# Kernel optimization log

Hardware: AMD Instinct MI355X
Metric: run time of the kernel (lower is better)

The kernel has to match this reference:

```python
import jax, jax.numpy as jnp
import numpy as np
from jax import lax

SOFTPLUS_THRESHOLD = 20.0

def _softplus_thresh(z):
    # softplus(z, beta=1, threshold=20): linear above threshold
    return jnp.where(z > SOFTPLUS_THRESHOLD, z,
                     jnp.log1p(jnp.exp(jnp.minimum(z, SOFTPLUS_THRESHOLD))))

def setup_inputs() -> dict:
    key = jax.random.key(0)
    ks = jax.random.split(key, 8)
    L, E, R, N = 512, 5120, 160, 16
    scale = 0.02
    x = jax.random.normal(ks[0], (1, 1, L, E), dtype=jnp.float32)
    W_dt_low = jax.random.normal(ks[1], (E, R), dtype=jnp.float32) * scale
    W_dt = jax.random.normal(ks[2], (R, E), dtype=jnp.float32) * scale
    dt_bias = jax.random.normal(ks[3], (E,), dtype=jnp.float32) * scale
    W_B = jax.random.normal(ks[4], (E, N), dtype=jnp.float32) * scale
    W_C = jax.random.normal(ks[5], (E, N), dtype=jnp.float32) * scale
    # A_log ~ log of positive values so A = -exp(A_log) is a stable decay
    A_log = jnp.log(1.0 + jax.random.uniform(ks[6], (E, N), dtype=jnp.float32) * 15.0)
    D = jax.random.normal(ks[7], (E,), dtype=jnp.float32)
    return {"x": x, "W_dt_low": W_dt_low, "W_dt": W_dt, "dt_bias": dt_bias,
            "W_B": W_B, "W_C": W_C, "A_log": A_log, "D": D}

def reference(x, W_dt_low, W_dt, dt_bias, W_B, W_C, A_log, D):
    orig_shape = x.shape              # [1,1,L,E]
    L, E = orig_shape[-2], orig_shape[-1]
    xf = x.reshape(L, E)
    # delta_t: x -> dt_rank -> d_inner, then thresholded softplus
    delta = _softplus_thresh((xf @ W_dt_low) @ W_dt + dt_bias)   # [L,E]
    A = -jnp.exp(A_log)                                          # [E,N]
    # discretization: abar = exp(delta * A), bbar = delta * B * x
    abar = jnp.exp(delta[:, :, None] * A[None])                  # [L,E,N]
    B = xf @ W_B                                                 # [L,N]
    bbar = delta[:, :, None] * B[:, None, :] * xf[:, :, None]    # [L,E,N]
    # linear recurrence h_t = abar_t * h_{t-1} + bbar_t via associative scan
    def combine(c1, c2):
        a1, b1 = c1
        a2, b2 = c2
        return a1 * a2, a2 * b1 + b2
    _, h = lax.associative_scan(combine, (abar, bbar), axis=0)   # [L,E,N]
    C = xf @ W_C                                                 # [L,N]
    y = jnp.einsum('len,ln->le', h, C)                           # hc_sum_reduce
    out = xf * D + y
    return out.reshape(orig_shape)
```

## Files before the change

### kernel.cpp

```cpp
#include <hip/hip_runtime.h>
#include <math.h>

#define LL 512
#define EE 5120
#define RR 160
#define NS 16
#define NTOT 192
#define KS 32
#define KCHUNK 160
#define CH 16
#define NC 32

#define XCONV_BLOCKS 1280
#define WALL_TILES   960
#define WDT_TILES    800

typedef __attribute__((ext_vector_type(8))) short short8;
typedef __attribute__((ext_vector_type(4))) short short4v;
typedef __attribute__((ext_vector_type(4))) float f32x4;

__device__ inline float softplus_t(float z) {
    return z > 20.f ? z : log1pf(__expf(fminf(z, 20.f)));
}

__device__ inline short f2bf(float f) {
    unsigned u = __float_as_uint(f);
    unsigned r = (u + 0x7FFFu + ((u >> 16) & 1u)) >> 16;
    return (short)r;
}

__device__ inline float bf2f(unsigned short u) {
    return __uint_as_float(((unsigned)u) << 16);
}

__global__ __launch_bounds__(256) void prep_kernel(
        const float* __restrict__ x,
        const float* __restrict__ Wlow,
        const float* __restrict__ WB,
        const float* __restrict__ WC,
        const float* __restrict__ Wdt,
        short* __restrict__ xb,
        short* __restrict__ WallT,
        short* __restrict__ WdtT) {
    const int tid = threadIdx.x;
    const int bid = blockIdx.x;
    if (bid < XCONV_BLOCKS) {
        size_t base = (size_t)bid * 2048 + (size_t)tid * 8;
        float4 v0 = *reinterpret_cast<const float4*>(x + base);
        float4 v1 = *reinterpret_cast<const float4*>(x + base + 4);
        short8 o;
        o[0] = f2bf(v0.x); o[1] = f2bf(v0.y); o[2] = f2bf(v0.z); o[3] = f2bf(v0.w);
        o[4] = f2bf(v1.x); o[5] = f2bf(v1.y); o[6] = f2bf(v1.z); o[7] = f2bf(v1.w);
        *reinterpret_cast<short8*>(xb + base) = o;
        return;
    }
    __shared__ float tile[32][33];
    const int row = tid >> 3, col4 = (tid & 7) * 4;
    if (bid < XCONV_BLOCKS + WALL_TILES) {
        const int t = bid - XCONV_BLOCKS;
        const int k0 = (t / 6) * 32, n0 = (t % 6) * 32;
#pragma unroll
        for (int i = 0; i < 4; ++i) {
            int n = n0 + col4 + i, k = k0 + row;
            float v;
            if (n < RR)            v = Wlow[(size_t)k * RR + n];
            else if (n < RR + NS)  v = WB[(size_t)k * NS + (n - RR)];
            else                   v = WC[(size_t)k * NS + (n - RR - NS)];
            tile[row][col4 + i] = v;
        }
        __syncthreads();
        const int nr = tid >> 3, kc = (tid & 7) * 4;
        short4v o;
#pragma unroll
        for (int i = 0; i < 4; ++i) o[i] = f2bf(tile[kc + i][nr]);
        *reinterpret_cast<short4v*>(WallT + (size_t)(n0 + nr) * EE + k0 + kc) = o;
    } else {
        const int t = bid - XCONV_BLOCKS - WALL_TILES;
        const int n0 = (t / 5) * 32, k0 = (t % 5) * 32;
#pragma unroll
        for (int i = 0; i < 4; ++i)
            tile[row][col4 + i] = Wdt[(size_t)(k0 + row) * EE + n0 + col4 + i];
        __syncthreads();
        const int nr = tid >> 3, kc = (tid & 7) * 4;
        short4v o;
#pragma unroll
        for (int i = 0; i < 4; ++i) o[i] = f2bf(tile[kc + i][nr]);
        *reinterpret_cast<short4v*>(WdtT + (size_t)(n0 + nr) * RR + k0 + kc) = o;
    }
}

__global__ __launch_bounds__(256) void g1m_kernel(
        const short* __restrict__ xb,
        const short* __restrict__ WallT,
        float* __restrict__ part) {
    const int tid = threadIdx.x;
    const int w = tid >> 6, l = tid & 63;
    const int wm = w >> 1, wn = w & 1;
    const int m0 = blockIdx.x * 64 + wm * 32;
    const int n0 = blockIdx.y * 64 + wn * 32;
    const int kz = blockIdx.z;
    const int row16 = l & 15, kg = (l >> 4) * 8;
    f32x4 acc[2][2] = {};
    const short* ap0 = xb + (size_t)(m0 + row16) * EE + kz * KCHUNK + kg;
    const short* ap1 = ap0 + (size_t)16 * EE;
    const short* bp0 = WallT + (size_t)(n0 + row16) * EE + kz * KCHUNK + kg;
    const short* bp1 = bp0 + (size_t)16 * EE;
#pragma unroll
    for (int s = 0; s < KCHUNK / 32; ++s) {
        short8 a0 = *reinterpret_cast<const short8*>(ap0 + s * 32);
        short8 a1 = *reinterpret_cast<const short8*>(ap1 + s * 32);
        short8 b0 = *reinterpret_cast<const short8*>(bp0 + s * 32);
        short8 b1 = *reinterpret_cast<const short8*>(bp1 + s * 32);
        acc[0][0] = __builtin_amdgcn_mfma_f32_16x16x32_bf16(a0, b0, acc[0][0], 0, 0, 0);
        acc[0][1] = __builtin_amdgcn_mfma_f32_16x16x32_bf16(a0, b1, acc[0][1], 0, 0, 0);
        acc[1][0] = __builtin_amdgcn_mfma_f32_16x16x32_bf16(a1, b0, acc[1][0], 0, 0, 0);
        acc[1][1] = __builtin_amdgcn_mfma_f32_16x16x32_bf16(a1, b1, acc[1][1], 0, 0, 0);
    }
    const int r0 = (l >> 4) * 4;
    const int c = l & 15;
#pragma unroll
    for (int i = 0; i < 2; ++i)
#pragma unroll
        for (int j = 0; j < 2; ++j) {
            size_t base = ((size_t)kz * LL + (m0 + i * 16 + r0)) * NTOT + (n0 + j * 16 + c);
            part[base]            = acc[i][j][0];
            part[base + NTOT]     = acc[i][j][1];
            part[base + 2 * NTOT] = acc[i][j][2];
            part[base + 3 * NTOT] = acc[i][j][3];
        }
}

__global__ __launch_bounds__(256) void r1_kernel(
        const float* __restrict__ part,
        short* __restrict__ tmpb,
        float* __restrict__ Bb,
        float* __restrict__ Cb) {
    int idx = blockIdx.x * 256 + threadIdx.x;
    int m = idx / NTOT, j = idx % NTOT;
    float s = 0.f;
#pragma unroll
    for (int ks = 0; ks < KS; ++ks) s += part[(size_t)ks * LL * NTOT + idx];
    if (j < RR) tmpb[m * RR + j] = f2bf(s);
    else if (j < RR + NS) Bb[m * NS + (j - RR)] = s;
    else Cb[m * NS + (j - RR - NS)] = s;
}

__global__ __launch_bounds__(256) void g2m_kernel(
        const short* __restrict__ tmpb,
        const short* __restrict__ WdtT,
        const float* __restrict__ bias,
        unsigned short* __restrict__ deltab) {
    const int tid = threadIdx.x;
    const int w = tid >> 6, l = tid & 63;
    const int wm = w >> 1, wn = w & 1;
    const int m0 = blockIdx.x * 64 + wm * 32;
    const int n0 = blockIdx.y * 64 + wn * 32;
    const int row16 = l & 15, koff = (l >> 4) * 8;
    f32x4 acc[2][2] = {};
    const short* aptr0 = tmpb + (size_t)(m0 + row16) * RR + koff;
    const short* aptr1 = aptr0 + (size_t)16 * RR;
    const short* bptr0 = WdtT + (size_t)(n0 + row16) * RR + koff;
    const short* bptr1 = bptr0 + (size_t)16 * RR;
#pragma unroll
    for (int s = 0; s < 5; ++s) {
        short8 a0 = *reinterpret_cast<const short8*>(aptr0 + s * 32);
        short8 a1 = *reinterpret_cast<const short8*>(aptr1 + s * 32);
        short8 b0 = *reinterpret_cast<const short8*>(bptr0 + s * 32);
        short8 b1 = *reinterpret_cast<const short8*>(bptr1 + s * 32);
        acc[0][0] = __builtin_amdgcn_mfma_f32_16x16x32_bf16(a0, b0, acc[0][0], 0, 0, 0);
        acc[0][1] = __builtin_amdgcn_mfma_f32_16x16x32_bf16(a0, b1, acc[0][1], 0, 0, 0);
        acc[1][0] = __builtin_amdgcn_mfma_f32_16x16x32_bf16(a1, b0, acc[1][0], 0, 0, 0);
        acc[1][1] = __builtin_amdgcn_mfma_f32_16x16x32_bf16(a1, b1, acc[1][1], 0, 0, 0);
    }
    const int r0 = (l >> 4) * 4;
    const int c = l & 15;
#pragma unroll
    for (int i = 0; i < 2; ++i) {
        int m = m0 + i * 16 + r0;
#pragma unroll
        for (int j = 0; j < 2; ++j) {
            int n = n0 + j * 16 + c;
            float bv = bias[n];
#pragma unroll
            for (int r = 0; r < 4; ++r)
                deltab[(size_t)(m + r) * EE + n] =
                    (unsigned short)f2bf(softplus_t(acc[i][j][r] + bv));
        }
    }
}

__global__ __launch_bounds__(256) void passA_kernel(
        const unsigned short* __restrict__ deltab,
        const unsigned short* __restrict__ xb,
        const float* __restrict__ Bb,
        const float* __restrict__ A_log,
        unsigned short* __restrict__ Hloc,
        float* __restrict__ sumd) {
    __shared__ float b_lds[CH][NS];
    const int c = blockIdx.y;
    const int e = blockIdx.x * 256 + threadIdx.x;
    const int t0 = c * CH;
    for (int v = threadIdx.x; v < CH * NS; v += 256)
        b_lds[v >> 4][v & 15] = Bb[t0 * NS + v];
    __syncthreads();

    float Ac[NS];
#pragma unroll
    for (int q = 0; q < 4; ++q) {
        float4 al = *reinterpret_cast<const float4*>(&A_log[(size_t)e * NS + q * 4]);
        Ac[q * 4 + 0] = -__expf(al.x);
        Ac[q * 4 + 1] = -__expf(al.y);
        Ac[q * 4 + 2] = -__expf(al.z);
        Ac[q * 4 + 3] = -__expf(al.w);
    }
    float h[NS];
#pragma unroll
    for (int n = 0; n < NS; ++n) h[n] = 0.f;
    float sd = 0.f;

#pragma unroll
    for (int tt = 0; tt < CH; ++tt) {
        float d  = bf2f(deltab[(size_t)(t0 + tt) * EE + e]);
        float xv = bf2f(xb[(size_t)(t0 + tt) * EE + e]);
        sd += d;
        float bx = d * xv;
#pragma unroll
        for (int n = 0; n < NS; ++n) {
            float a = __expf(d * Ac[n]);
            h[n] = a * h[n] + bx * b_lds[tt][n];
        }
    }
    size_t base = ((size_t)c * EE + e) * NS;
    short8 p0, p1;
#pragma unroll
    for (int n = 0; n < 8; ++n) { p0[n] = f2bf(h[n]); p1[n] = f2bf(h[n + 8]); }
    *reinterpret_cast<short8*>(Hloc + base)     = p0;
    *reinterpret_cast<short8*>(Hloc + base + 8) = p1;
    sumd[(size_t)c * EE + e] = sd;
}

__global__ __launch_bounds__(256) void passB_kernel(
        const unsigned short* __restrict__ Hloc,
        const float* __restrict__ sumd,
        const float* __restrict__ A_log,
        unsigned short* __restrict__ Hstart) {
    const int wk = blockIdx.x * 256 + threadIdx.x;
    const int eB = wk >> 4;
    const float AcB = -__expf(A_log[wk]);
    float hs = 0.f;
#pragma unroll
    for (int cc = 0; cc < NC; ++cc) {
        size_t off = (size_t)cc * EE * NS + wk;
        Hstart[off] = (unsigned short)f2bf(hs);
        hs = __expf(AcB * sumd[(size_t)cc * EE + eB]) * hs + bf2f(Hloc[off]);
    }
}

__global__ __launch_bounds__(256) void passC_kernel(
        const unsigned short* __restrict__ deltab,
        const unsigned short* __restrict__ xb,
        const float* __restrict__ Bb,
        const float* __restrict__ Cb,
        const float* __restrict__ A_log,
        const float* __restrict__ Dvec,
        const unsigned short* __restrict__ Hstart,
        float* __restrict__ out) {
    __shared__ float b_lds[CH][NS];
    __shared__ float c_lds[CH][NS];
    const int c = blockIdx.y;
    const int e = blockIdx.x * 256 + threadIdx.x;
    const int t0 = c * CH;
    for (int v = threadIdx.x; v < CH * NS; v += 256) {
        b_lds[v >> 4][v & 15] = Bb[t0 * NS + v];
        c_lds[v >> 4][v & 15] = Cb[t0 * NS + v];
    }
    __syncthreads();

    float Ac[NS];
#pragma unroll
    for (int q = 0; q < 4; ++q) {
        float4 al = *reinterpret_cast<const float4*>(&A_log[(size_t)e * NS + q * 4]);
        Ac[q * 4 + 0] = -__expf(al.x);
        Ac[q * 4 + 1] = -__expf(al.y);
        Ac[q * 4 + 2] = -__expf(al.z);
        Ac[q * 4 + 3] = -__expf(al.w);
    }
    float h[NS];
    size_t base = ((size_t)c * EE + e) * NS;
    {
        short8 p0 = *reinterpret_cast<const short8*>(Hstart + base);
        short8 p1 = *reinterpret_cast<const short8*>(Hstart + base + 8);
#pragma unroll
        for (int n = 0; n < 8; ++n) {
            h[n]     = bf2f((unsigned short)p0[n]);
            h[n + 8] = bf2f((unsigned short)p1[n]);
        }
    }
    const float Dval = Dvec[e];

#pragma unroll
    for (int tt = 0; tt < CH; ++tt) {
        float d  = bf2f(deltab[(size_t)(t0 + tt) * EE + e]);
        float xv = bf2f(xb[(size_t)(t0 + tt) * EE + e]);
        float bx = d * xv;
        float y = 0.f;
#pragma unroll
        for (int n = 0; n < NS; ++n) {
            float a = __expf(d * Ac[n]);
            h[n] = a * h[n] + bx * b_lds[tt][n];
            y += h[n] * c_lds[tt][n];
        }
        out[(size_t)(t0 + tt) * EE + e] = xv * Dval + y;
    }
}

extern "C" void kernel_launch(void* const* d_in, const int* in_sizes, int n_in,
                              void* d_out, int out_size, void* d_ws, size_t ws_size,
                              hipStream_t stream) {
    const float* x     = (const float*)d_in[0];
    const float* Wlow  = (const float*)d_in[1];
    const float* Wdt   = (const float*)d_in[2];
    const float* bias  = (const float*)d_in[3];
    const float* WB    = (const float*)d_in[4];
    const float* WC    = (const float*)d_in[5];
    const float* Alog  = (const float*)d_in[6];
    const float* Dv    = (const float*)d_in[7];
    float* out = (float*)d_out;
    float* wsf = (float*)d_ws;

    float*          Bb     = wsf;
    float*          Cb     = wsf + 8192;
    short*          WallT  = (short*)(wsf + 16384);
    short*          WdtT   = (short*)(wsf + 507904);
    short*          tmpb   = (short*)(wsf + 917504);
    short*          xb     = (short*)(wsf + 958464);
    float*          part   = wsf + 2269184;
    unsigned short* deltab = (unsigned short*)(wsf + 5414912);
    unsigned short* Hloc   = (unsigned short*)(wsf + 6725632);
    unsigned short* Hstart = (unsigned short*)(wsf + 8036352);
    float*          sumd   = wsf + 9347072;

    prep_kernel<<<dim3(XCONV_BLOCKS + WALL_TILES + WDT_TILES), 256, 0, stream>>>(
        x, Wlow, WB, WC, Wdt, xb, WallT, WdtT);
    g1m_kernel<<<dim3(8, 3, KS), 256, 0, stream>>>(xb, WallT, part);
    r1_kernel<<<dim3(384), 256, 0, stream>>>(part, tmpb, Bb, Cb);
    g2m_kernel<<<dim3(8, 80), 256, 0, stream>>>(tmpb, WdtT, bias, deltab);
    passA_kernel<<<dim3(EE / 256, NC), 256, 0, stream>>>(
        deltab, (const unsigned short*)xb, Bb, Alog, Hloc, sumd);
    passB_kernel<<<dim3((EE * NS) / 256), 256, 0, stream>>>(Hloc, sumd, Alog, Hstart);
    passC_kernel<<<dim3(EE / 256, NC), 256, 0, stream>>>(
        deltab, (const unsigned short*)xb, Bb, Cb, Alog, Dv, Hstart, out);
}
```

Measured before the change: 70.82 us.

## Fuse delta GEMM into scan passes and fold chunk-carry scan into passC

Removes the separate g2m kernel and the deltab buffer: each scan block recomputes its 32x256 delta tile with MFMA into LDS, in both passA and passC. The passB carry kernel is dropped, and each passC block instead serially combines the Hloc/sumd of all previous chunks itself. Chunk size doubles to 32 and the chunk count halves to 16. This saves two launches and the delta round-trip through global memory, at the cost of computing the delta GEMM twice, a prefix loop of up to 15 steps per thread in passC, and half as many blocks per scan pass.

```diff
diff --git a/kernel.cpp b/kernel.cpp
--- a/kernel.cpp
+++ b/kernel.cpp
@@ -8,8 +8,9 @@
 #define NTOT 192
 #define KS 32
 #define KCHUNK 160
-#define CH 16
-#define NC 32
+#define CH 32
+#define NC 16
+#define DPAD 258
 
 #define XCONV_BLOCKS 1280
 #define WALL_TILES   960
@@ -145,65 +146,68 @@
     else Cb[m * NS + (j - RR - NS)] = s;
 }
 
-__global__ __launch_bounds__(256) void g2m_kernel(
+__device__ inline void delta_tile_mfma(
         const short* __restrict__ tmpb,
         const short* __restrict__ WdtT,
         const float* __restrict__ bias,
-        unsigned short* __restrict__ deltab) {
-    const int tid = threadIdx.x;
+        int c, int e0, int tid,
+        float (*d_lds)[DPAD]) {
     const int w = tid >> 6, l = tid & 63;
-    const int wm = w >> 1, wn = w & 1;
-    const int m0 = blockIdx.x * 64 + wm * 32;
-    const int n0 = blockIdx.y * 64 + wn * 32;
     const int row16 = l & 15, koff = (l >> 4) * 8;
-    f32x4 acc[2][2] = {};
-    const short* aptr0 = tmpb + (size_t)(m0 + row16) * RR + koff;
-    const short* aptr1 = aptr0 + (size_t)16 * RR;
-    const short* bptr0 = WdtT + (size_t)(n0 + row16) * RR + koff;
-    const short* bptr1 = bptr0 + (size_t)16 * RR;
+    const int t0 = c * CH;
+    f32x4 acc[2][4] = {};
+    const short* ap0 = tmpb + (size_t)(t0 + row16) * RR + koff;
+    const short* ap1 = ap0 + (size_t)16 * RR;
+    const short* bpw = WdtT + (size_t)(e0 + w * 64 + row16) * RR + koff;
 #pragma unroll
     for (int s = 0; s < 5; ++s) {
-        short8 a0 = *reinterpret_cast<const short8*>(aptr0 + s * 32);
-        short8 a1 = *reinterpret_cast<const short8*>(aptr1 + s * 32);
-        short8 b0 = *reinterpret_cast<const short8*>(bptr0 + s * 32);
-        short8 b1 = *reinterpret_cast<const short8*>(bptr1 + s * 32);
-        acc[0][0] = __builtin_amdgcn_mfma_f32_16x16x32_bf16(a0, b0, acc[0][0], 0, 0, 0);
-        acc[0][1] = __builtin_amdgcn_mfma_f32_16x16x32_bf16(a0, b1, acc[0][1], 0, 0, 0);
-        acc[1][0] = __builtin_amdgcn_mfma_f32_16x16x32_bf16(a1, b0, acc[1][0], 0, 0, 0);
-        acc[1][1] = __builtin_amdgcn_mfma_f32_16x16x32_bf16(a1, b1, acc[1][1], 0, 0, 0);
-    }
+        short8 a0 = *reinterpret_cast<const short8*>(ap0 + s * 32);
+        short8 a1 = *reinterpret_cast<const short8*>(ap1 + s * 32);
+#pragma unroll
+        for (int nf = 0; nf < 4; ++nf) {
+            short8 b = *reinterpret_cast<const short8*>(bpw + (size_t)nf * 16 * RR + s * 32);
+            acc[0][nf] = __builtin_amdgcn_mfma_f32_16x16x32_bf16(a0, b, acc[0][nf], 0, 0, 0);
+            acc[1][nf] = __builtin_amdgcn_mfma_f32_16x16x32_bf16(a1, b, acc[1][nf], 0, 0, 0);
+        }
+    }
+    const int col = l & 15;
     const int r0 = (l >> 4) * 4;
-    const int c = l & 15;
-#pragma unroll
-    for (int i = 0; i < 2; ++i) {
-        int m = m0 + i * 16 + r0;
-#pragma unroll
-        for (int j = 0; j < 2; ++j) {
-            int n = n0 + j * 16 + c;
-            float bv = bias[n];
+#pragma unroll
+    for (int nf = 0; nf < 4; ++nf) {
+        int el = w * 64 + nf * 16 + col;
+        float bv = bias[e0 + el];
+#pragma unroll
+        for (int mf = 0; mf < 2; ++mf) {
 #pragma unroll
             for (int r = 0; r < 4; ++r)
-                deltab[(size_t)(m + r) * EE + n] =
-                    (unsigned short)f2bf(softplus_t(acc[i][j][r] + bv));
+                d_lds[mf * 16 + r0 + r][el] = softplus_t(acc[mf][nf][r] + bv);
         }
     }
 }
 
 __global__ __launch_bounds__(256) void passA_kernel(
-        const unsigned short* __restrict__ deltab,
+        const short* __restrict__ tmpb,
+        const short* __restrict__ WdtT,
+        const float* __restrict__ bias,
         const unsigned short* __restrict__ xb,
         const float* __restrict__ Bb,
         const float* __restrict__ A_log,
         unsigned short* __restrict__ Hloc,
         float* __restrict__ sumd) {
+    __shared__ float d_lds[CH][DPAD];
     __shared__ float b_lds[CH][NS];
     const int c = blockIdx.y;
-    const int e = blockIdx.x * 256 + threadIdx.x;
+    const int e0 = blockIdx.x * 256;
+    const int tid = threadIdx.x;
     const int t0 = c * CH;
-    for (int v = threadIdx.x; v < CH * NS; v += 256)
+
+    for (int v = tid; v < CH * NS; v += 256)
         b_lds[v >> 4][v & 15] = Bb[t0 * NS + v];
+
+    delta_tile_mfma(tmpb, WdtT, bias, c, e0, tid, d_lds);
     __syncthreads();
 
+    const int e = e0 + tid;
     float Ac[NS];
 #pragma unroll
     for (int q = 0; q < 4; ++q) {
@@ -218,9 +222,9 @@
     for (int n = 0; n < NS; ++n) h[n] = 0.f;
     float sd = 0.f;
 
-#pragma unroll
+#pragma unroll 8
     for (int tt = 0; tt < CH; ++tt) {
-        float d  = bf2f(deltab[(size_t)(t0 + tt) * EE + e]);
+        float d  = d_lds[tt][tid];
         float xv = bf2f(xb[(size_t)(t0 + tt) * EE + e]);
         sd += d;
         float bx = d * xv;
@@ -239,43 +243,35 @@
     sumd[(size_t)c * EE + e] = sd;
 }
 
-__global__ __launch_bounds__(256) void passB_kernel(
-        const unsigned short* __restrict__ Hloc,
-        const float* __restrict__ sumd,
-        const float* __restrict__ A_log,
-        unsigned short* __restrict__ Hstart) {
-    const int wk = blockIdx.x * 256 + threadIdx.x;
-    const int eB = wk >> 4;
-    const float AcB = -__expf(A_log[wk]);
-    float hs = 0.f;
-#pragma unroll
-    for (int cc = 0; cc < NC; ++cc) {
-        size_t off = (size_t)cc * EE * NS + wk;
-        Hstart[off] = (unsigned short)f2bf(hs);
-        hs = __expf(AcB * sumd[(size_t)cc * EE + eB]) * hs + bf2f(Hloc[off]);
-    }
-}
-
 __global__ __launch_bounds__(256) void passC_kernel(
-        const unsigned short* __restrict__ deltab,
+        const short* __restrict__ tmpb,
+        const short* __restrict__ WdtT,
+        const float* __restrict__ bias,
         const unsigned short* __restrict__ xb,
         const float* __restrict__ Bb,
         const float* __restrict__ Cb,
         const float* __restrict__ A_log,
         const float* __restrict__ Dvec,
-        const unsigned short* __restrict__ Hstart,
+        const unsigned short* __restrict__ Hloc,
+        const float* __restrict__ sumd,
         float* __restrict__ out) {
+    __shared__ float d_lds[CH][DPAD];
     __shared__ float b_lds[CH][NS];
     __shared__ float c_lds[CH][NS];
     const int c = blockIdx.y;
-    const int e = blockIdx.x * 256 + threadIdx.x;
+    const int e0 = blockIdx.x * 256;
+    const int tid = threadIdx.x;
     const int t0 = c * CH;
-    for (int v = threadIdx.x; v < CH * NS; v += 256) {
+
+    for (int v = tid; v < CH * NS; v += 256) {
         b_lds[v >> 4][v & 15] = Bb[t0 * NS + v];
         c_lds[v >> 4][v & 15] = Cb[t0 * NS + v];
     }
+
+    delta_tile_mfma(tmpb, WdtT, bias, c, e0, tid, d_lds);
     __syncthreads();
 
+    const int e = e0 + tid;
     float Ac[NS];
 #pragma unroll
     for (int q = 0; q < 4; ++q) {
@@ -285,22 +281,26 @@
         Ac[q * 4 + 2] = -__expf(al.z);
         Ac[q * 4 + 3] = -__expf(al.w);
     }
+
     float h[NS];
-    size_t base = ((size_t)c * EE + e) * NS;
-    {
-        short8 p0 = *reinterpret_cast<const short8*>(Hstart + base);
-        short8 p1 = *reinterpret_cast<const short8*>(Hstart + base + 8);
+#pragma unroll
+    for (int n = 0; n < NS; ++n) h[n] = 0.f;
+    for (int cc = 0; cc < c; ++cc) {
+        float sdc = sumd[(size_t)cc * EE + e];
+        size_t off = ((size_t)cc * EE + e) * NS;
+        short8 p0 = *reinterpret_cast<const short8*>(Hloc + off);
+        short8 p1 = *reinterpret_cast<const short8*>(Hloc + off + 8);
 #pragma unroll
         for (int n = 0; n < 8; ++n) {
-            h[n]     = bf2f((unsigned short)p0[n]);
-            h[n + 8] = bf2f((unsigned short)p1[n]);
-        }
-    }
+            h[n]     = __expf(Ac[n] * sdc)     * h[n]     + bf2f((unsigned short)p0[n]);
+            h[n + 8] = __expf(Ac[n + 8] * sdc) * h[n + 8] + bf2f((unsigned short)p1[n]);
+        }
+    }
+
     const float Dval = Dvec[e];
-
-#pragma unroll
+#pragma unroll 8
     for (int tt = 0; tt < CH; ++tt) {
-        float d  = bf2f(deltab[(size_t)(t0 + tt) * EE + e]);
+        float d  = d_lds[tt][tid];
         float xv = bf2f(xb[(size_t)(t0 + tt) * EE + e]);
         float bx = d * xv;
         float y = 0.f;
@@ -328,26 +328,23 @@
     float* out = (float*)d_out;
     float* wsf = (float*)d_ws;
 
-    float*          Bb     = wsf;
-    float*          Cb     = wsf + 8192;
-    short*          WallT  = (short*)(wsf + 16384);
-    short*          WdtT   = (short*)(wsf + 507904);
-    short*          tmpb   = (short*)(wsf + 917504);
-    short*          xb     = (short*)(wsf + 958464);
-    float*          part   = wsf + 2269184;
-    unsigned short* deltab = (unsigned short*)(wsf + 5414912);
-    unsigned short* Hloc   = (unsigned short*)(wsf + 6725632);
-    unsigned short* Hstart = (unsigned short*)(wsf + 8036352);
-    float*          sumd   = wsf + 9347072;
+    float*          Bb    = wsf;
+    float*          Cb    = wsf + 8192;
+    short*          WallT = (short*)(wsf + 16384);
+    short*          WdtT  = (short*)(wsf + 507904);
+    short*          tmpb  = (short*)(wsf + 917504);
+    short*          xb    = (short*)(wsf + 958464);
+    float*          part  = wsf + 2269184;
+    unsigned short* Hloc  = (unsigned short*)(wsf + 5414912);
+    float*          sumd  = wsf + 6070272;
 
     prep_kernel<<<dim3(XCONV_BLOCKS + WALL_TILES + WDT_TILES), 256, 0, stream>>>(
         x, Wlow, WB, WC, Wdt, xb, WallT, WdtT);
     g1m_kernel<<<dim3(8, 3, KS), 256, 0, stream>>>(xb, WallT, part);
     r1_kernel<<<dim3(384), 256, 0, stream>>>(part, tmpb, Bb, Cb);
-    g2m_kernel<<<dim3(8, 80), 256, 0, stream>>>(tmpb, WdtT, bias, deltab);
     passA_kernel<<<dim3(EE / 256, NC), 256, 0, stream>>>(
-        deltab, (const unsigned short*)xb, Bb, Alog, Hloc, sumd);
-    passB_kernel<<<dim3((EE * NS) / 256), 256, 0, stream>>>(Hloc, sumd, Alog, Hstart);
+        tmpb, WdtT, bias, (const unsigned short*)xb, Bb, Alog, Hloc, sumd);
     passC_kernel<<<dim3(EE / 256, NC), 256, 0, stream>>>(
-        deltab, (const unsigned short*)xb, Bb, Cb, Alog, Dv, Hstart, out);
-}
+        tmpb, WdtT, bias, (const unsigned short*)xb, Bb, Cb, Alog, Dv,
+        Hloc, sumd, out);
+}
```

Result: slower. 112.1 us (+58.4%).
